# Optimization experiments

Measured on AMD Instinct MI355X. Metric: run time of the kernel, lower is better.

The kernel has to match this reference:

```python
import jax, jax.numpy as jnp
import numpy as np

B, S, D, H = 2, 2048, 1024, 16
HD = D // H  # head_dim = 64


def setup_inputs() -> dict:
    key = jax.random.key(0)
    ks = jax.random.split(key, 5)
    scale = 0.02
    x = jax.random.normal(ks[0], (B, S, D), dtype=jnp.float32)
    Wq = scale * jax.random.normal(ks[1], (H, D, HD), dtype=jnp.float32)
    Wk = scale * jax.random.normal(ks[2], (H, D, HD), dtype=jnp.float32)
    Wv = scale * jax.random.normal(ks[3], (H, D, HD), dtype=jnp.float32)
    Wo = scale * jax.random.normal(ks[4], (D, D), dtype=jnp.float32)
    bq = jnp.zeros((H, HD), dtype=jnp.float32)
    bk = jnp.zeros((H, HD), dtype=jnp.float32)
    bv = jnp.zeros((H, HD), dtype=jnp.float32)
    bo = jnp.zeros((D,), dtype=jnp.float32)
    return {"x": x, "Wq": Wq, "bq": bq, "Wk": Wk, "bk": bk,
            "Wv": Wv, "bv": bv, "Wo": Wo, "bo": bo}


def reference(x, Wq, bq, Wk, bk, Wv, bv, Wo, bo):
    # Per-head QKV projections (the torch module's per-head nn.Linear list,
    # vectorized over the head axis h). Dropout is identity (eval mode).
    q = jnp.einsum("bsd,hde->bhse", x, Wq) + bq[None, :, None, :]  # [B,H,S,HD]
    k = jnp.einsum("bsd,hde->bhse", x, Wk) + bk[None, :, None, :]
    v = jnp.einsum("bsd,hde->bhse", x, Wv) + bv[None, :, None, :]

    norm = jnp.asarray(np.sqrt(HD), dtype=x.dtype)
    scores = jnp.einsum("bhse,bhte->bhst", q, k) / norm  # [B,H,S,S]
    causal = jnp.tril(jnp.ones((S, S), dtype=bool))
    scores = jnp.where(causal[None, None], scores, jnp.asarray(-jnp.inf, dtype=scores.dtype))
    attn = jax.nn.softmax(scores, axis=-1)

    wv = jnp.einsum("bhst,bhte->bhse", attn, v)          # [B,H,S,HD]
    wv = jnp.transpose(wv, (0, 2, 1, 3)).reshape(B, S, D)  # concat heads on last dim
    out = wv @ Wo.T + bo                                   # output projection
    return out
```

## Files before the change

### kernel.cpp

```cpp
#include <hip/hip_runtime.h>


#define DD 1024
#define SS 2048
#define BB 2
#define HH 16
#define HD 64
#define QSCALE 0.18033688011112042f
#define LSTR 88

typedef __attribute__((ext_vector_type(8))) short short8;
typedef __attribute__((ext_vector_type(4))) float float4v;
typedef unsigned short ushort;
typedef unsigned int uint;

__device__ inline ushort f2bf(float f) {
    union { float f; uint i; } v; v.f = f;
    uint r = v.i + 0x7FFF + ((v.i >> 16) & 1);
    return (ushort)(r >> 16);
}
__device__ inline ushort f2bf_f(float f) {
    union { float f; uint i; } v; v.f = f;
    return (ushort)((v.i + 0x8000u) >> 16);
}
__device__ inline uint pack_bf2(float a, float b) {
    return (uint)f2bf_f(a) | ((uint)f2bf_f(b) << 16);
}

__device__ __forceinline__ void cp16(const ushort* g, ushort* l) {
    __builtin_amdgcn_global_load_lds((const __attribute__((address_space(1))) void*)g,
                                     (__attribute__((address_space(3))) void*)l,
                                     16, 0, 0);
}

__global__ __launch_bounds__(256) void prep(const float* __restrict__ x,
                                            const float* __restrict__ Wo,
                                            const float* __restrict__ Wq,
                                            const float* __restrict__ Wk,
                                            const float* __restrict__ Wv,
                                            ushort* __restrict__ xb,
                                            ushort* __restrict__ Wob,
                                            ushort* __restrict__ W3T) {
    __shared__ ushort T[64][65];
    int bid = blockIdx.x, t = threadIdx.x;
    if (bid < 5120) {
        const float* src; ushort* dst; int j;
        if (bid < 4096) { src = x;  dst = xb;  j = bid * 256 + t; }
        else            { src = Wo; dst = Wob; j = (bid - 4096) * 256 + t; }
        float4 v = ((const float4*)src)[j];
        ushort o[4] = { f2bf(v.x), f2bf(v.y), f2bf(v.z), f2bf(v.w) };
        ((uint2*)dst)[j] = *(const uint2*)o;
        return;
    }
    int i = bid - 5120;
    int z = i >> 8, h = (i >> 4) & 15, d0 = (i & 15) * 64;
    const float* W = z == 0 ? Wq : (z == 1 ? Wk : Wv);
    const float* Wh = W + h * DD * HD;
    ushort* Wt = W3T + ((size_t)z * HH + h) * HD * DD;
    #pragma unroll
    for (int s = 0; s < 4; s++) {
        int idx = t + s * 256;
        int d = idx >> 4, e4 = (idx & 15) * 4;
        float4 v = *(const float4*)(Wh + (d0 + d) * HD + e4);
        T[d][e4 + 0] = f2bf(v.x); T[d][e4 + 1] = f2bf(v.y);
        T[d][e4 + 2] = f2bf(v.z); T[d][e4 + 3] = f2bf(v.w);
    }
    __syncthreads();
    #pragma unroll
    for (int s = 0; s < 2; s++) {
        int idx = t + s * 256;
        int e = idx >> 3, d8 = (idx & 7) * 8;
        ushort tmp[8];
        #pragma unroll
        for (int j = 0; j < 8; j++) tmp[j] = T[d8 + j][e];
        *(uint4*)(Wt + e * DD + d0 + d8) = *(uint4*)tmp;
    }
}

__global__ __launch_bounds__(256) void gemm_qkv(const ushort* __restrict__ xb,
                                                const ushort* __restrict__ W3T,
                                                const float* __restrict__ bq,
                                                const float* __restrict__ bk,
                                                const float* __restrict__ bv,
                                                ushort* __restrict__ qb,
                                                ushort* __restrict__ kb,
                                                ushort* __restrict__ vT) {
    __shared__ ushort Al[128 * 64];
    __shared__ ushort Bl[3][64 * 64];
    int m0 = blockIdx.x * 128, n0 = blockIdx.y * 64;
    int t = threadIdx.x, lane = t & 63, w = t >> 6;
    int wm = w & 1, wn = w >> 1;
    int qm = lane >> 4, lm = lane & 15;

    const ushort* W0 = W3T + (size_t)n0 * DD;
    const ushort* W1 = W3T + (size_t)(HH * HD + n0) * DD;
    const ushort* W2 = W3T + (size_t)(2 * HH * HD + n0) * DD;

    float4v acc[3][4][2] = {};
    for (int k0 = 0; k0 < DD; k0 += 64) {
        __syncthreads();
        #pragma unroll
        for (int s = 0; s < 4; s++) {
            int c = t + s * 256;
            int row = c >> 3;
            int j = (c & 7) ^ (row & 7);
            cp16(xb + (size_t)(m0 + row) * DD + k0 + j * 8, Al + c * 8);
        }
        #pragma unroll
        for (int s = 0; s < 2; s++) {
            int c = t + s * 256;
            int row = c >> 3;
            int j = (c & 7) ^ (row & 7);
            cp16(W0 + (size_t)row * DD + k0 + j * 8, Bl[0] + c * 8);
            cp16(W1 + (size_t)row * DD + k0 + j * 8, Bl[1] + c * 8);
            cp16(W2 + (size_t)row * DD + k0 + j * 8, Bl[2] + c * 8);
        }
        __syncthreads();
        #pragma unroll
        for (int h2 = 0; h2 < 2; h2++) {
            int sw = ((((h2 << 2) | qm) ^ (lm & 7)) << 3);
            short8 a[4];
            #pragma unroll
            for (int i = 0; i < 4; i++)
                a[i] = *(const short8*)(Al + ((wm * 64 + i * 16 + lm) << 6) + sw);
            #pragma unroll
            for (int z = 0; z < 3; z++) {
                short8 b0 = *(const short8*)(Bl[z] + ((wn * 32 + lm) << 6) + sw);
                short8 b1 = *(const short8*)(Bl[z] + ((wn * 32 + 16 + lm) << 6) + sw);
                if (z == 2) {
                    #pragma unroll
                    for (int i = 0; i < 4; i++) {
                        acc[2][i][0] = __builtin_amdgcn_mfma_f32_16x16x32_bf16(a[i], b0, acc[2][i][0], 0, 0, 0);
                        acc[2][i][1] = __builtin_amdgcn_mfma_f32_16x16x32_bf16(a[i], b1, acc[2][i][1], 0, 0, 0);
                    }
                } else {
                    #pragma unroll
                    for (int i = 0; i < 4; i++) {
                        acc[z][i][0] = __builtin_amdgcn_mfma_f32_16x16x32_bf16(b0, a[i], acc[z][i][0], 0, 0, 0);
                        acc[z][i][1] = __builtin_amdgcn_mfma_f32_16x16x32_bf16(b1, a[i], acc[z][i][1], 0, 0, 0);
                    }
                }
            }
        }
    }
    #pragma unroll
    for (int z = 0; z < 2; z++) {
        const float* bias = z == 0 ? bq : bk;
        ushort* Out = z == 0 ? qb : kb;
        float sc = z == 0 ? QSCALE : 1.0f;
        #pragma unroll
        for (int j = 0; j < 2; j++) {
            int nb = n0 + wn * 32 + j * 16 + qm * 4;
            float4 b4 = *(const float4*)(bias + nb);
            #pragma unroll
            for (int i = 0; i < 4; i++) {
                int m = m0 + wm * 64 + i * 16 + lm;
                uint2 o2;
                o2.x = pack_bf2((acc[z][i][j][0] + b4.x) * sc, (acc[z][i][j][1] + b4.y) * sc);
                o2.y = pack_bf2((acc[z][i][j][2] + b4.z) * sc, (acc[z][i][j][3] + b4.w) * sc);
                *(uint2*)(Out + (size_t)m * DD + nb) = o2;
            }
        }
    }
    #pragma unroll
    for (int j = 0; j < 2; j++) {
        int n = n0 + wn * 32 + j * 16 + lm;
        int h = n >> 6, e = n & 63;
        float bb = bv[n];
        #pragma unroll
        for (int i = 0; i < 4; i++) {
            int m = m0 + wm * 64 + i * 16 + qm * 4;
            int b_ = m >> 11, s = m & (SS - 1);
            uint2 o2;
            o2.x = pack_bf2(acc[2][i][j][0] + bb, acc[2][i][j][1] + bb);
            o2.y = pack_bf2(acc[2][i][j][2] + bb, acc[2][i][j][3] + bb);
            *(uint2*)(vT + ((size_t)(b_ * HH + h) * HD + e) * SS + s) = o2;
        }
    }
}

__global__ __launch_bounds__(512, 4) void attn(const ushort* __restrict__ Q,
                                               const ushort* __restrict__ K,
                                               const ushort* __restrict__ VT,
                                               ushort* __restrict__ O) {
    __shared__ ushort QP[128][LSTR];
    __shared__ ushort Kl[2][64][LSTR];
    __shared__ ushort Vl[2][64][LSTR];
    int bh = blockIdx.x, px = blockIdx.y;
    int qt = 15 - px;
    int b = bh >> 4, h = bh & 15;
    int m0 = qt * 128;
    int njt = 2 * (qt + 1);
    const ushort* Qp = Q + (size_t)b * SS * DD + h * HD;
    const ushort* Kp = K + (size_t)b * SS * DD + h * HD;
    const ushort* Vp = VT + (size_t)bh * HD * SS;
    int t = threadIdx.x, lane = t & 63, w = t >> 6;
    int qm = lane >> 4, lm = lane & 15;
    int row0 = t >> 3, colc = (t & 7) * 8;

    *(uint4*)(&QP[row0][colc])      = *(const uint4*)(Qp + (size_t)(m0 + row0) * DD + colc);
    *(uint4*)(&QP[row0 + 64][colc]) = *(const uint4*)(Qp + (size_t)(m0 + row0 + 64) * DD + colc);
    *(uint4*)(&Kl[0][row0][colc])   = *(const uint4*)(Kp + (size_t)row0 * DD + colc);
    *(uint4*)(&Vl[0][row0][colc])   = *(const uint4*)(Vp + (size_t)row0 * SS + colc);
    __syncthreads();

    short8 qf[2];
    qf[0] = *(const short8*)(&QP[w * 16 + lm][qm * 8]);
    qf[1] = *(const short8*)(&QP[w * 16 + lm][32 + qm * 8]);

    float4v o[4] = {};
    float li = 0.f;
    int cur = 0;
    int qg = m0 + w * 16 + lm;

    for (int jt = 0; jt < njt; jt++) {
        if (jt) __syncthreads();
        bool pre = jt + 1 < njt;
        uint4 pk, pv;
        if (pre) {
            int nn = (jt + 1) * 64;
            pk = *(const uint4*)(Kp + (size_t)(nn + row0) * DD + colc);
            pv = *(const uint4*)(Vp + (size_t)row0 * SS + nn + colc);
        }

        float4v s[4] = {};
        #pragma unroll
        for (int kc = 0; kc < 2; kc++) {
            #pragma unroll
            for (int j = 0; j < 4; j++) {
                short8 ak = *(const short8*)(&Kl[cur][j * 16 + lm][kc * 32 + qm * 8]);
                s[j] = __builtin_amdgcn_mfma_f32_16x16x32_bf16(ak, qf[kc], s[j], 0, 0, 0);
            }
        }
        if (jt >= 2 * qt) {
            #pragma unroll
            for (int j = 0; j < 4; j++)
                #pragma unroll
                for (int r = 0; r < 4; r++)
                    if (jt * 64 + j * 16 + qm * 4 + r > qg) s[j][r] = -__builtin_inff();
        }
        #pragma unroll
        for (int j = 0; j < 4; j++) {
            float p0 = __builtin_amdgcn_exp2f(s[j][0]);
            float p1 = __builtin_amdgcn_exp2f(s[j][1]);
            float p2 = __builtin_amdgcn_exp2f(s[j][2]);
            float p3 = __builtin_amdgcn_exp2f(s[j][3]);
            li += (p0 + p1) + (p2 + p3);
            uint2 u; u.x = pack_bf2(p0, p1); u.y = pack_bf2(p2, p3);
            *(uint2*)(&QP[w * 16 + lm][j * 16 + qm * 4]) = u;
        }
        asm volatile("s_waitcnt lgkmcnt(0)" ::: "memory");

        #pragma unroll
        for (int kc = 0; kc < 2; kc++) {
            short8 ap = *(const short8*)(&QP[w * 16 + lm][kc * 32 + qm * 8]);
            #pragma unroll
            for (int jn = 0; jn < 4; jn++) {
                short8 av = *(const short8*)(&Vl[cur][jn * 16 + lm][kc * 32 + qm * 8]);
                o[jn] = __builtin_amdgcn_mfma_f32_16x16x32_bf16(av, ap, o[jn], 0, 0, 0);
            }
        }
        if (pre) {
            *(uint4*)(&Kl[cur ^ 1][row0][colc]) = pk;
            *(uint4*)(&Vl[cur ^ 1][row0][colc]) = pv;
        }
        cur ^= 1;
    }
    li += __shfl_xor(li, 16, 64);
    li += __shfl_xor(li, 32, 64);
    float inv = 1.f / li;
    ushort* Ob = O + ((size_t)b * SS + qg) * DD + h * HD;
    #pragma unroll
    for (int jn = 0; jn < 4; jn++) {
        uint2 u;
        u.x = pack_bf2(o[jn][0] * inv, o[jn][1] * inv);
        u.y = pack_bf2(o[jn][2] * inv, o[jn][3] * inv);
        *(uint2*)(Ob + jn * 16 + qm * 4) = u;
    }
}

__global__ __launch_bounds__(256) void gemm_out(const ushort* __restrict__ X,
                                                const ushort* __restrict__ Wob,
                                                const float* __restrict__ bo,
                                                float* __restrict__ Out) {
    __shared__ ushort Al[128 * 64];
    __shared__ ushort Bl[64 * 64];
    int m0 = blockIdx.x * 128, n0 = blockIdx.y * 64;
    int t = threadIdx.x, lane = t & 63, w = t >> 6;
    int wm = w & 1, wn = w >> 1;
    int qm = lane >> 4, lm = lane & 15;

    float4v acc[4][2] = {};
    for (int k0 = 0; k0 < DD; k0 += 64) {
        __syncthreads();
        #pragma unroll
        for (int s = 0; s < 4; s++) {
            int c = t + s * 256;
            int row = c >> 3;
            int j = (c & 7) ^ (row & 7);
            cp16(X + (size_t)(m0 + row) * DD + k0 + j * 8, Al + c * 8);
        }
        #pragma unroll
        for (int s = 0; s < 2; s++) {
            int c = t + s * 256;
            int row = c >> 3;
            int j = (c & 7) ^ (row & 7);
            cp16(Wob + (size_t)(n0 + row) * DD + k0 + j * 8, Bl + c * 8);
        }
        __syncthreads();
        #pragma unroll
        for (int h2 = 0; h2 < 2; h2++) {
            int sw = ((((h2 << 2) | qm) ^ (lm & 7)) << 3);
            short8 a[4], b[2];
            #pragma unroll
            for (int i = 0; i < 4; i++)
                a[i] = *(const short8*)(Al + ((wm * 64 + i * 16 + lm) << 6) + sw);
            #pragma unroll
            for (int j = 0; j < 2; j++)
                b[j] = *(const short8*)(Bl + ((wn * 32 + j * 16 + lm) << 6) + sw);
            #pragma unroll
            for (int i = 0; i < 4; i++)
                #pragma unroll
                for (int j = 0; j < 2; j++)
                    acc[i][j] = __builtin_amdgcn_mfma_f32_16x16x32_bf16(b[j], a[i], acc[i][j], 0, 0, 0);
        }
    }
    #pragma unroll
    for (int j = 0; j < 2; j++) {
        int nb = n0 + wn * 32 + j * 16 + qm * 4;
        float4 b4 = *(const float4*)(bo + nb);
        #pragma unroll
        for (int i = 0; i < 4; i++) {
            int m = m0 + wm * 64 + i * 16 + lm;
            float4 st;
            st.x = acc[i][j][0] + b4.x;
            st.y = acc[i][j][1] + b4.y;
            st.z = acc[i][j][2] + b4.z;
            st.w = acc[i][j][3] + b4.w;
            *(float4*)(Out + (size_t)m * DD + nb) = st;
        }
    }
}

extern "C" void kernel_launch(void* const* d_in, const int* in_sizes, int n_in,
                              void* d_out, int out_size, void* d_ws, size_t ws_size,
                              hipStream_t stream) {
    const float* x   = (const float*)d_in[0];
    const float* Wq  = (const float*)d_in[1];
    const float* bq  = (const float*)d_in[2];
    const float* Wk  = (const float*)d_in[3];
    const float* bk  = (const float*)d_in[4];
    const float* Wv_ = (const float*)d_in[5];
    const float* bv  = (const float*)d_in[6];
    const float* Wo  = (const float*)d_in[7];
    const float* bo  = (const float*)d_in[8];
    float* out = (float*)d_out;

    ushort* xb  = (ushort*)d_ws;
    ushort* W3T = xb  + (size_t)BB * SS * DD;
    ushort* Wob = W3T + (size_t)3 * HH * HD * DD;
    ushort* qb  = Wob + (size_t)DD * DD;
    ushort* kb  = qb + (size_t)BB * SS * DD;
    ushort* vT  = kb + (size_t)BB * SS * DD;
    ushort* wvb = vT + (size_t)BB * SS * DD;

    prep<<<dim3(5888), 256, 0, stream>>>(x, Wo, Wq, Wk, Wv_, xb, Wob, W3T);
    gemm_qkv<<<dim3(32, 16), 256, 0, stream>>>(xb, W3T, bq, bk, bv, qb, kb, vT);
    attn<<<dim3(32, 16), 512, 0, stream>>>(qb, kb, vT, wvb);
    gemm_out<<<dim3(32, 16), 256, 0, stream>>>(wvb, Wob, bo, out);
}
```

Baseline: 181.8 us.

## Stream K/V tiles via direct global-to-LDS loads with XOR swizzle and interleaved block order

The attention kernel now stages K and V tiles with global_load_lds into unpadded, XOR-swizzled LDS buffers. This replaces register-staged loads followed by LDS stores, removing the register round-trip and shrinking LDS use. The grid becomes 1D and pairs long and short causal query tiles in launch order to balance work across CUs. Bf16 packing also switches to the hardware cvt_pk_bf16_f32 builtin when it is available, which changes rounding from round-half-up to the builtin's rounding.

```diff
diff --git a/kernel.cpp b/kernel.cpp
--- a/kernel.cpp
+++ b/kernel.cpp
@@ -19,13 +19,19 @@
     uint r = v.i + 0x7FFF + ((v.i >> 16) & 1);
     return (ushort)(r >> 16);
 }
-__device__ inline ushort f2bf_f(float f) {
-    union { float f; uint i; } v; v.f = f;
-    return (ushort)((v.i + 0x8000u) >> 16);
-}
+#if __has_builtin(__builtin_amdgcn_cvt_pk_bf16_f32)
+typedef __bf16 bf16x2 __attribute__((ext_vector_type(2)));
 __device__ inline uint pack_bf2(float a, float b) {
-    return (uint)f2bf_f(a) | ((uint)f2bf_f(b) << 16);
-}
+    union { bf16x2 v; uint u; } c;
+    c.v = __builtin_amdgcn_cvt_pk_bf16_f32(a, b);
+    return c.u;
+}
+#else
+__device__ inline uint pack_bf2(float a, float b) {
+    union { float f; uint i; } x, y; x.f = a; y.f = b;
+    return ((x.i + 0x8000u) >> 16) | (((y.i + 0x8000u) >> 16) << 16);
+}
+#endif
 
 __device__ __forceinline__ void cp16(const ushort* g, ushort* l) {
     __builtin_amdgcn_global_load_lds((const __attribute__((address_space(1))) void*)g,
@@ -184,10 +190,12 @@
                                                const ushort* __restrict__ VT,
                                                ushort* __restrict__ O) {
     __shared__ ushort QP[128][LSTR];
-    __shared__ ushort Kl[2][64][LSTR];
-    __shared__ ushort Vl[2][64][LSTR];
-    int bh = blockIdx.x, px = blockIdx.y;
-    int qt = 15 - px;
+    __shared__ ushort Kl[2][64 * 64];
+    __shared__ ushort Vl[2][64 * 64];
+    int id = blockIdx.x;
+    int bh = id & 31;
+    int j5 = (id >> 5) & 7;
+    int qt = (id < 256) ? (15 - 2 * j5) : (2 * j5);
     int b = bh >> 4, h = bh & 15;
     int m0 = qt * 128;
     int njt = 2 * (qt + 1);
@@ -197,11 +205,13 @@
     int t = threadIdx.x, lane = t & 63, w = t >> 6;
     int qm = lane >> 4, lm = lane & 15;
     int row0 = t >> 3, colc = (t & 7) * 8;
+    int srow = t >> 3;
+    int sj = (t & 7) ^ (srow & 7);
 
     *(uint4*)(&QP[row0][colc])      = *(const uint4*)(Qp + (size_t)(m0 + row0) * DD + colc);
     *(uint4*)(&QP[row0 + 64][colc]) = *(const uint4*)(Qp + (size_t)(m0 + row0 + 64) * DD + colc);
-    *(uint4*)(&Kl[0][row0][colc])   = *(const uint4*)(Kp + (size_t)row0 * DD + colc);
-    *(uint4*)(&Vl[0][row0][colc])   = *(const uint4*)(Vp + (size_t)row0 * SS + colc);
+    cp16(Kp + (size_t)srow * DD + sj * 8, Kl[0] + t * 8);
+    cp16(Vp + (size_t)srow * SS + sj * 8, Vl[0] + t * 8);
     __syncthreads();
 
     short8 qf[2];
@@ -212,25 +222,24 @@
     float li = 0.f;
     int cur = 0;
     int qg = m0 + w * 16 + lm;
+    int swz = ((qm ^ (lm & 7)) << 3);
+    int swz1 = (((4 | qm) ^ (lm & 7)) << 3);
 
     for (int jt = 0; jt < njt; jt++) {
         if (jt) __syncthreads();
-        bool pre = jt + 1 < njt;
-        uint4 pk, pv;
-        if (pre) {
+        if (jt + 1 < njt) {
             int nn = (jt + 1) * 64;
-            pk = *(const uint4*)(Kp + (size_t)(nn + row0) * DD + colc);
-            pv = *(const uint4*)(Vp + (size_t)row0 * SS + nn + colc);
+            cp16(Kp + (size_t)(nn + srow) * DD + sj * 8, Kl[cur ^ 1] + t * 8);
+            cp16(Vp + (size_t)srow * SS + nn + sj * 8, Vl[cur ^ 1] + t * 8);
         }
 
         float4v s[4] = {};
         #pragma unroll
-        for (int kc = 0; kc < 2; kc++) {
-            #pragma unroll
-            for (int j = 0; j < 4; j++) {
-                short8 ak = *(const short8*)(&Kl[cur][j * 16 + lm][kc * 32 + qm * 8]);
-                s[j] = __builtin_amdgcn_mfma_f32_16x16x32_bf16(ak, qf[kc], s[j], 0, 0, 0);
-            }
+        for (int j = 0; j < 4; j++) {
+            short8 ak0 = *(const short8*)(Kl[cur] + ((j * 16 + lm) << 6) + swz);
+            short8 ak1 = *(const short8*)(Kl[cur] + ((j * 16 + lm) << 6) + swz1);
+            s[j] = __builtin_amdgcn_mfma_f32_16x16x32_bf16(ak0, qf[0], s[j], 0, 0, 0);
+            s[j] = __builtin_amdgcn_mfma_f32_16x16x32_bf16(ak1, qf[1], s[j], 0, 0, 0);
         }
         if (jt >= 2 * qt) {
             #pragma unroll
@@ -254,15 +263,12 @@
         #pragma unroll
         for (int kc = 0; kc < 2; kc++) {
             short8 ap = *(const short8*)(&QP[w * 16 + lm][kc * 32 + qm * 8]);
+            int so = kc ? swz1 : swz;
             #pragma unroll
             for (int jn = 0; jn < 4; jn++) {
-                short8 av = *(const short8*)(&Vl[cur][jn * 16 + lm][kc * 32 + qm * 8]);
+                short8 av = *(const short8*)(Vl[cur] + ((jn * 16 + lm) << 6) + so);
                 o[jn] = __builtin_amdgcn_mfma_f32_16x16x32_bf16(av, ap, o[jn], 0, 0, 0);
             }
-        }
-        if (pre) {
-            *(uint4*)(&Kl[cur ^ 1][row0][colc]) = pk;
-            *(uint4*)(&Vl[cur ^ 1][row0][colc]) = pv;
         }
         cur ^= 1;
     }
@@ -366,6 +372,6 @@
 
     prep<<<dim3(5888), 256, 0, stream>>>(x, Wo, Wq, Wk, Wv_, xb, Wob, W3T);
     gemm_qkv<<<dim3(32, 16), 256, 0, stream>>>(xb, W3T, bq, bk, bv, qb, kb, vT);
-    attn<<<dim3(32, 16), 512, 0, stream>>>(qb, kb, vT, wvb);
+    attn<<<dim3(512), 512, 0, stream>>>(qb, kb, vT, wvb);
     gemm_out<<<dim3(32, 16), 256, 0, stream>>>(wvb, Wob, bo, out);
 }
```

Result: no change. 180.7 us (-0.6%).
